# Optimization experiments

Hardware: AMD Instinct MI355X
Metric: run time of the kernel (lower is better)

## Reference

```python
import math
import jax, jax.numpy as jnp
import numpy as np

C = 32        # per-head dim
N_HEAD = 8
C_IN = 128

def setup_inputs() -> dict:
    key = jax.random.key(0)
    ks = jax.random.split(key, 10)
    B, S = 1, 256
    sc = 0.05  # keep logits in a sane range
    x    = jax.random.normal(ks[0], (B, S, S, C_IN), dtype=jnp.float32)
    bias = jax.random.normal(ks[1], (B, N_HEAD, S, S), dtype=jnp.float32)
    attention_mask = jax.random.randint(ks[2], (B, S, S), 0, 2).astype(bool)
    Wq = jax.random.normal(ks[3], (C_IN, C * N_HEAD), dtype=jnp.float32) * sc
    Wk = jax.random.normal(ks[4], (C_IN, C * N_HEAD), dtype=jnp.float32) * sc
    Wv = jax.random.normal(ks[5], (C_IN, C * N_HEAD), dtype=jnp.float32) * sc
    Wo = jax.random.normal(ks[6], (C * N_HEAD, C_IN), dtype=jnp.float32) * sc
    bo = jnp.zeros((C_IN,), dtype=jnp.float32)
    Wg = jax.random.normal(ks[7], (C_IN, C * N_HEAD), dtype=jnp.float32) * sc
    bg = jnp.zeros((C * N_HEAD,), dtype=jnp.float32)
    return {"x": x, "bias": bias, "attention_mask": attention_mask,
            "Wq": Wq, "Wk": Wk, "Wv": Wv, "Wo": Wo, "bo": bo, "Wg": Wg, "bg": bg}

def reference(x, bias, attention_mask, Wq, Wk, Wv, Wo, bo, Wg, bg):
    # x: [B, S, L, c_in]; attn_dim=2 is already the second-to-last dim,
    # so the torch movedim(attn_dim, -2) is the identity here.
    B, S, L, _ = x.shape
    q = x @ Wq  # [B, S, L, H*c]
    k = x @ Wk
    v = x @ Wv
    # split heads: [B, S, L, H, c] -> [B, S, H, L, c]
    def split_heads(t):
        return t.reshape(B, S, L, N_HEAD, C).transpose(0, 1, 3, 2, 4)
    q, k, v = split_heads(q), split_heads(k), split_heads(v)
    q = q / math.sqrt(C)
    # attention logits: [B, S, H, q, k]
    a = jnp.einsum('bshqc,bshkc->bshqk', q, k)
    # bias [B, H, q, k] -> broadcast over the axial batch dim S
    a = a + bias[:, None, :, :, :]
    # mask [B, S, k] -> [B, S, 1, 1, k]; masked positions get -inf
    m = attention_mask[:, :, None, None, :]
    a = jnp.where(m, a, -jnp.inf)
    a = jax.nn.softmax(a, axis=-1)
    o = jnp.einsum('bshqk,bshkc->bshqc', a, v)
    # merge heads: [B, S, H, L, c] -> [B, S, L, H*c]
    o = o.transpose(0, 1, 3, 2, 4).reshape(B, S, L, N_HEAD * C)
    # sigmoid gate
    g = jax.nn.sigmoid(x @ Wg + bg)
    o = g * o
    return o @ Wo + bo
```

## Files before the change

### kernel.cpp

```cpp
#include <hip/hip_runtime.h>
#include <hip/hip_bf16.h>
#include <cstdint>

#define CIN 128
#define NH 8
#define CH 32

typedef short bf16x8 __attribute__((ext_vector_type(8)));
typedef short bf16x4 __attribute__((ext_vector_type(4)));
typedef float f32x4 __attribute__((ext_vector_type(4)));

__device__ __forceinline__ short f2bf(float f) {
  union { float f; unsigned u; } v; v.f = f;
  unsigned r = (v.u + 0x7FFFu + ((v.u >> 16) & 1u)) >> 16;
  return (short)r;
}
__device__ __forceinline__ float bf2f(short s) {
  union { unsigned u; float f; } v; v.u = ((unsigned)(unsigned short)s) << 16;
  return v.f;
}
__device__ __forceinline__ unsigned pk2bf(float a, float b) {
  union { __hip_bfloat162 h; unsigned u; } cv;
  cv.h = __float22bfloat162_rn(make_float2(a, b));
  return cv.u;
}

__global__ __launch_bounds__(256) void prep(
    const float* __restrict__ Wq, const float* __restrict__ Wk,
    const float* __restrict__ Wv, const float* __restrict__ Wg,
    const float* __restrict__ Wo,
    const uint4* __restrict__ mask,
    short* __restrict__ WT, short* __restrict__ WoT,
    unsigned int* __restrict__ flag)
{
  __shared__ int viol;
  const int b = blockIdx.x;
  if (b < 64) {
    const float qscale = 0.17677669529663689f;
#pragma unroll
    for (int e = 0; e < 10; ++e) {
      int o = b * 2560 + e * 256 + threadIdx.x;
      if (o < 131072) {
        int n = o >> 7, k = o & 127;
        int seg = n >> 8, nn = n & 255;
        const float* W = (seg == 0) ? Wq : (seg == 1) ? Wk : (seg == 2) ? Wv : Wg;
        float v = W[k * 256 + nn];
        if (seg == 0) v *= qscale;
        WT[o] = f2bf(v);
      } else {
        int o2 = o - 131072;
        int n = o2 >> 8, k = o2 & 255;
        WoT[o2] = f2bf(Wo[k * 128 + n]);
      }
    }
  } else {
    if (threadIdx.x == 0) viol = 0;
    __syncthreads();
    int v = 0;
#pragma unroll
    for (int j = 0; j < 16; ++j) {
      uint4 w = mask[j * 256 + threadIdx.x];
      v |= (w.x > 1u) | (w.y > 1u) | (w.z > 1u) | (w.w > 1u);
    }
    if (v) atomicOr(&viol, 1);
    __syncthreads();
    if (threadIdx.x == 0) *flag = viol ? 0u : 1u;
  }
}

__global__ __launch_bounds__(512) void fused_attn(
    const float* __restrict__ x, const short* __restrict__ WT,
    const float* __restrict__ bias, const float* __restrict__ bg,
    const void* __restrict__ maskraw, const unsigned int* __restrict__ flagp,
    short* __restrict__ og)
{
  __shared__ __align__(16) short xl[256 * 136];
  __shared__ __align__(16) short kL[256 * 40];
  __shared__ __align__(16) short vL[32 * 264];
  __shared__ __align__(16) short qL[256 * 40];
  __shared__ __align__(16) short gL[256 * 40];
  __shared__ float lL[256];
  __shared__ unsigned int scratch[8];

  const int tid = threadIdx.x;
  const int srow = blockIdx.x;
  const int lane = tid & 63, w = tid >> 6;
  const int g = lane >> 4, c16 = lane & 15;
  const int myrow = w * 32;

  const unsigned int fl = *flagp;
  if (tid < 256) {
    int mv = fl ? ((const int*)maskraw)[srow * 256 + tid]
                : (int)((const unsigned char*)maskraw)[srow * 256 + tid];
    unsigned long long bb = __ballot(mv != 0);
    if (lane == 0) {
      scratch[w * 2 + 0] = (unsigned int)bb;
      scratch[w * 2 + 1] = (unsigned int)(bb >> 32);
    }
  }

  {
    const float* xs = x + (size_t)srow * 256 * 128;
#pragma unroll
    for (int it = 0; it < 16; ++it) {
      int idx = it * 512 + tid;
      int row = idx >> 5, c4 = idx & 31;
      float4 a = *(const float4*)(xs + (size_t)idx * 4);
      union { unsigned u[2]; bf16x4 v; } pu;
      pu.u[0] = pk2bf(a.x, a.y);
      pu.u[1] = pk2bf(a.z, a.w);
      *(bf16x4*)&xl[row * 136 + c4 * 4] = pu.v;
    }
  }
  __syncthreads();

  unsigned int mb[8];
#pragma unroll
  for (int j = 0; j < 8; ++j) mb[j] = scratch[j];

  const f32x4 zero4 = {0.f, 0.f, 0.f, 0.f};

#pragma unroll 1
  for (int h = 0; h < 8; ++h) {
    {
      f32x4 acc[2][2];
#pragma unroll
      for (int ct = 0; ct < 2; ++ct)
#pragma unroll
        for (int rt = 0; rt < 2; ++rt) acc[ct][rt] = zero4;
#pragma unroll
      for (int kk = 0; kk < 4; ++kk) {
        bf16x8 wf[2], xf[2];
#pragma unroll
        for (int ct = 0; ct < 2; ++ct)
          wf[ct] = *(const bf16x8*)(WT + (size_t)(256 + h * CH + ct * 16 + c16) * 128 + kk * 32 + g * 8);
#pragma unroll
        for (int rt = 0; rt < 2; ++rt)
          xf[rt] = *(const bf16x8*)&xl[(myrow + rt * 16 + c16) * 136 + kk * 32 + g * 8];
#pragma unroll
        for (int ct = 0; ct < 2; ++ct)
#pragma unroll
          for (int rt = 0; rt < 2; ++rt)
            acc[ct][rt] = __builtin_amdgcn_mfma_f32_16x16x32_bf16(wf[ct], xf[rt], acc[ct][rt], 0, 0, 0);
      }
#pragma unroll
      for (int ct = 0; ct < 2; ++ct)
#pragma unroll
        for (int rt = 0; rt < 2; ++rt) {
          union { unsigned u[2]; bf16x4 v; } pu;
          pu.u[0] = pk2bf(acc[ct][rt][0], acc[ct][rt][1]);
          pu.u[1] = pk2bf(acc[ct][rt][2], acc[ct][rt][3]);
          *(bf16x4*)&kL[(myrow + rt * 16 + c16) * 40 + ct * 16 + g * 4] = pu.v;
        }
    }
    {
      f32x4 acc[2][2];
#pragma unroll
      for (int rt = 0; rt < 2; ++rt)
#pragma unroll
        for (int ct = 0; ct < 2; ++ct) acc[rt][ct] = zero4;
#pragma unroll
      for (int kk = 0; kk < 4; ++kk) {
        bf16x8 wf[2], xf[2];
#pragma unroll
        for (int ct = 0; ct < 2; ++ct)
          wf[ct] = *(const bf16x8*)(WT + (size_t)(512 + h * CH + ct * 16 + c16) * 128 + kk * 32 + g * 8);
#pragma unroll
        for (int rt = 0; rt < 2; ++rt)
          xf[rt] = *(const bf16x8*)&xl[(myrow + rt * 16 + c16) * 136 + kk * 32 + g * 8];
#pragma unroll
        for (int rt = 0; rt < 2; ++rt)
#pragma unroll
          for (int ct = 0; ct < 2; ++ct)
            acc[rt][ct] = __builtin_amdgcn_mfma_f32_16x16x32_bf16(xf[rt], wf[ct], acc[rt][ct], 0, 0, 0);
      }
#pragma unroll
      for (int rt = 0; rt < 2; ++rt)
#pragma unroll
        for (int ct = 0; ct < 2; ++ct) {
          union { unsigned u[2]; bf16x4 v; } pu;
          pu.u[0] = pk2bf(acc[rt][ct][0], acc[rt][ct][1]);
          pu.u[1] = pk2bf(acc[rt][ct][2], acc[rt][ct][3]);
          *(bf16x4*)&vL[(ct * 16 + c16) * 264 + myrow + rt * 16 + g * 4] = pu.v;
        }
    }
    {
      f32x4 acc[2][2];
#pragma unroll
      for (int ct = 0; ct < 2; ++ct)
#pragma unroll
        for (int rt = 0; rt < 2; ++rt) acc[ct][rt] = zero4;
#pragma unroll
      for (int kk = 0; kk < 4; ++kk) {
        bf16x8 wf[2], xf[2];
#pragma unroll
        for (int ct = 0; ct < 2; ++ct)
          wf[ct] = *(const bf16x8*)(WT + (size_t)(0 + h * CH + ct * 16 + c16) * 128 + kk * 32 + g * 8);
#pragma unroll
        for (int rt = 0; rt < 2; ++rt)
          xf[rt] = *(const bf16x8*)&xl[(myrow + rt * 16 + c16) * 136 + kk * 32 + g * 8];
#pragma unroll
        for (int ct = 0; ct < 2; ++ct)
#pragma unroll
          for (int rt = 0; rt < 2; ++rt)
            acc[ct][rt] = __builtin_amdgcn_mfma_f32_16x16x32_bf16(wf[ct], xf[rt], acc[ct][rt], 0, 0, 0);
      }
#pragma unroll
      for (int ct = 0; ct < 2; ++ct)
#pragma unroll
        for (int rt = 0; rt < 2; ++rt) {
          union { unsigned u[2]; bf16x4 v; } pu;
          pu.u[0] = pk2bf(acc[ct][rt][0], acc[ct][rt][1]);
          pu.u[1] = pk2bf(acc[ct][rt][2], acc[ct][rt][3]);
          *(bf16x4*)&qL[(myrow + rt * 16 + c16) * 40 + ct * 16 + g * 4] = pu.v;
        }
    }
    {
      f32x4 acc[2][2];
#pragma unroll
      for (int ct = 0; ct < 2; ++ct)
#pragma unroll
        for (int rt = 0; rt < 2; ++rt) acc[ct][rt] = zero4;
#pragma unroll
      for (int kk = 0; kk < 4; ++kk) {
        bf16x8 wf[2], xf[2];
#pragma unroll
        for (int ct = 0; ct < 2; ++ct)
          wf[ct] = *(const bf16x8*)(WT + (size_t)(768 + h * CH + ct * 16 + c16) * 128 + kk * 32 + g * 8);
#pragma unroll
        for (int rt = 0; rt < 2; ++rt)
          xf[rt] = *(const bf16x8*)&xl[(myrow + rt * 16 + c16) * 136 + kk * 32 + g * 8];
#pragma unroll
        for (int ct = 0; ct < 2; ++ct)
#pragma unroll
          for (int rt = 0; rt < 2; ++rt)
            acc[ct][rt] = __builtin_amdgcn_mfma_f32_16x16x32_bf16(wf[ct], xf[rt], acc[ct][rt], 0, 0, 0);
      }
#pragma unroll
      for (int ct = 0; ct < 2; ++ct) {
        float4 bgv = *(const float4*)(bg + h * CH + ct * 16 + g * 4);
#pragma unroll
        for (int rt = 0; rt < 2; ++rt) {
          float v0 = 1.f / (1.f + __expf(-(acc[ct][rt][0] + bgv.x)));
          float v1 = 1.f / (1.f + __expf(-(acc[ct][rt][1] + bgv.y)));
          float v2 = 1.f / (1.f + __expf(-(acc[ct][rt][2] + bgv.z)));
          float v3 = 1.f / (1.f + __expf(-(acc[ct][rt][3] + bgv.w)));
          union { unsigned u[2]; bf16x4 v; } pu;
          pu.u[0] = pk2bf(v0, v1);
          pu.u[1] = pk2bf(v2, v3);
          *(bf16x4*)&gL[(myrow + rt * 16 + c16) * 40 + ct * 16 + g * 4] = pu.v;
        }
      }
    }
    __syncthreads();

    const int qb = myrow;
    bf16x8 qf[2];
#pragma unroll
    for (int qt = 0; qt < 2; ++qt)
      qf[qt] = *(const bf16x8*)&qL[(qb + qt * 16 + c16) * 40 + g * 8];

    float l_[2] = {0.f, 0.f};
    f32x4 O[2][2];
#pragma unroll
    for (int qt = 0; qt < 2; ++qt) { O[qt][0] = zero4; O[qt][1] = zero4; }

    const float* bh = bias + (size_t)h * 65536;

#pragma unroll 1
    for (int ch = 0; ch < 8; ++ch) {
      float4 bb4[2][2];
#pragma unroll
      for (int kt = 0; kt < 2; ++kt)
#pragma unroll
        for (int qt = 0; qt < 2; ++qt)
          bb4[kt][qt] = *(const float4*)(bh + (size_t)(qb + qt * 16 + c16) * 256 +
                                         ch * 32 + kt * 16 + g * 4);

#pragma unroll
      for (int kt = 0; kt < 2; ++kt) {
        bf16x8 kf = *(const bf16x8*)&kL[(ch * 32 + kt * 16 + c16) * 40 + g * 8];
        bf16x4 vlo = *(const bf16x4*)&vL[(size_t)c16 * 264 + ch * 32 + kt * 16 + g * 4];
        bf16x4 vhi = *(const bf16x4*)&vL[(size_t)(16 + c16) * 264 + ch * 32 + kt * 16 + g * 4];
        const unsigned nib = (mb[ch] >> (kt * 16 + g * 4)) & 0xFu;
        float em[4];
#pragma unroll
        for (int i = 0; i < 4; ++i) em[i] = ((nib >> i) & 1u) ? 1.f : 0.f;
#pragma unroll
        for (int qt = 0; qt < 2; ++qt) {
          f32x4 S = __builtin_amdgcn_mfma_f32_16x16x32_bf16(kf, qf[qt], zero4, 0, 0, 0);
          float p0 = em[0] * __expf(fminf(S[0] + bb4[kt][qt].x, 85.f));
          float p1 = em[1] * __expf(fminf(S[1] + bb4[kt][qt].y, 85.f));
          float p2 = em[2] * __expf(fminf(S[2] + bb4[kt][qt].z, 85.f));
          float p3 = em[3] * __expf(fminf(S[3] + bb4[kt][qt].w, 85.f));
          l_[qt] += (p0 + p1) + (p2 + p3);
          union { unsigned u[2]; bf16x4 v; } pu;
          pu.u[0] = pk2bf(p0, p1);
          pu.u[1] = pk2bf(p2, p3);
          O[qt][0] = __builtin_amdgcn_mfma_f32_16x16x16bf16_1k(pu.v, vlo, O[qt][0], 0, 0, 0);
          O[qt][1] = __builtin_amdgcn_mfma_f32_16x16x16bf16_1k(pu.v, vhi, O[qt][1], 0, 0, 0);
        }
      }
    }

#pragma unroll
    for (int qt = 0; qt < 2; ++qt) {
      float v = l_[qt];
      v += __shfl_xor(v, 16);
      v += __shfl_xor(v, 32);
      if (lane < 16) lL[myrow + qt * 16 + c16] = v;
    }

#pragma unroll
    for (int qt = 0; qt < 2; ++qt)
#pragma unroll
      for (int i = 0; i < 4; ++i) {
        float l = lL[myrow + qt * 16 + g * 4 + i];
        float inv = 1.f / l;
        int row = qb + qt * 16 + g * 4 + i;
        short* orow = og + ((size_t)srow * 256 + row) * 256 + h * CH;
#pragma unroll
        for (int half = 0; half < 2; ++half) {
          int c = half * 16 + c16;
          float gv = bf2f(gL[row * 40 + c]);
          orow[c] = f2bf(O[qt][half][i] * inv * gv);
        }
      }
    __syncthreads();
  }
}

__global__ __launch_bounds__(256) void out_proj(
    const short* __restrict__ og, const short* __restrict__ WoT,
    const float* __restrict__ bo, float* __restrict__ out)
{
  __shared__ short Al[64 * 136];
  __shared__ short Bl[128 * 136];
  const int tid = threadIdx.x;
  const int lane = tid & 63, w = tid >> 6;
  const int g = lane >> 4, c16 = lane & 15;
  const int wr = w & 1, wc = w >> 1;
  const int row0 = blockIdx.x * 64;

  f32x4 acc[2][4];
#pragma unroll
  for (int rt = 0; rt < 2; ++rt)
#pragma unroll
    for (int ct = 0; ct < 4; ++ct) acc[rt][ct] = (f32x4){0.f, 0.f, 0.f, 0.f};

  for (int kk0 = 0; kk0 < 256; kk0 += 128) {
#pragma unroll
    for (int ch = 0; ch < 4; ++ch) {
      int c = ch * 256 + tid;
      int r = c >> 4, kc = c & 15;
      *(bf16x8*)&Al[r * 136 + kc * 8] =
          *(const bf16x8*)(og + (size_t)(row0 + r) * 256 + kk0 + kc * 8);
    }
#pragma unroll
    for (int ch = 0; ch < 8; ++ch) {
      int c = ch * 256 + tid;
      int r = c >> 4, kc = c & 15;
      *(bf16x8*)&Bl[r * 136 + kc * 8] =
          *(const bf16x8*)(WoT + (size_t)r * 256 + kk0 + kc * 8);
    }
    __syncthreads();
#pragma unroll
    for (int kk = 0; kk < 4; ++kk) {
      bf16x8 af[2], bfr[4];
#pragma unroll
      for (int rt = 0; rt < 2; ++rt)
        af[rt] = *(const bf16x8*)&Al[(wr * 32 + rt * 16 + c16) * 136 + kk * 32 + g * 8];
#pragma unroll
      for (int ct = 0; ct < 4; ++ct)
        bfr[ct] = *(const bf16x8*)&Bl[(wc * 64 + ct * 16 + c16) * 136 + kk * 32 + g * 8];
#pragma unroll
      for (int rt = 0; rt < 2; ++rt)
#pragma unroll
        for (int ct = 0; ct < 4; ++ct)
          acc[rt][ct] = __builtin_amdgcn_mfma_f32_16x16x32_bf16(af[rt], bfr[ct], acc[rt][ct], 0, 0, 0);
    }
    __syncthreads();
  }

#pragma unroll
  for (int rt = 0; rt < 2; ++rt)
#pragma unroll
    for (int ct = 0; ct < 4; ++ct) {
      int col = wc * 64 + ct * 16 + c16;
      float bv = bo[col];
#pragma unroll
      for (int i = 0; i < 4; ++i) {
        int row = row0 + wr * 32 + rt * 16 + g * 4 + i;
        out[(size_t)row * CIN + col] = acc[rt][ct][i] + bv;
      }
    }
}

extern "C" void kernel_launch(void* const* d_in, const int* in_sizes, int n_in,
                              void* d_out, int out_size, void* d_ws, size_t ws_size,
                              hipStream_t stream) {
  const float* x    = (const float*)d_in[0];
  const float* bias = (const float*)d_in[1];
  const void*  mask = d_in[2];
  const float* Wq   = (const float*)d_in[3];
  const float* Wk   = (const float*)d_in[4];
  const float* Wv   = (const float*)d_in[5];
  const float* Wo   = (const float*)d_in[6];
  const float* bo   = (const float*)d_in[7];
  const float* Wg   = (const float*)d_in[8];
  const float* bg   = (const float*)d_in[9];
  float* out = (float*)d_out;

  unsigned int* flag = (unsigned int*)d_ws;
  short* WT  = (short*)((char*)d_ws + 256);
  short* WoT = WT + 131072;
  short* og  = WoT + 32768;

  prep<<<65, 256, 0, stream>>>(Wq, Wk, Wv, Wg, Wo, (const uint4*)mask,
                               WT, WoT, flag);
  fused_attn<<<256, 512, 0, stream>>>(x, WT, bias, bg, mask, flag, og);
  out_proj<<<1024, 256, 0, stream>>>(og, WoT, bo, out);
}
```

Measured before the change: 245.7 us.

## Fuse output projection into attention kernel, accumulating per-head Wo contributions

```diff
diff --git a/kernel.cpp b/kernel.cpp
--- a/kernel.cpp
+++ b/kernel.cpp
@@ -70,15 +70,16 @@
 
 __global__ __launch_bounds__(512) void fused_attn(
     const float* __restrict__ x, const short* __restrict__ WT,
+    const short* __restrict__ WoT,
     const float* __restrict__ bias, const float* __restrict__ bg,
+    const float* __restrict__ bo,
     const void* __restrict__ maskraw, const unsigned int* __restrict__ flagp,
-    short* __restrict__ og)
+    float* __restrict__ out)
 {
   __shared__ __align__(16) short xl[256 * 136];
   __shared__ __align__(16) short kL[256 * 40];
   __shared__ __align__(16) short vL[32 * 264];
   __shared__ __align__(16) short qL[256 * 40];
-  __shared__ __align__(16) short gL[256 * 40];
   __shared__ float lL[256];
   __shared__ unsigned int scratch[8];
 
@@ -119,9 +120,15 @@
   for (int j = 0; j < 8; ++j) mb[j] = scratch[j];
 
   const f32x4 zero4 = {0.f, 0.f, 0.f, 0.f};
+  f32x4 acc_out[2][8];
+#pragma unroll
+  for (int qt = 0; qt < 2; ++qt)
+#pragma unroll
+    for (int ct = 0; ct < 8; ++ct) acc_out[qt][ct] = zero4;
 
 #pragma unroll 1
   for (int h = 0; h < 8; ++h) {
+    f32x4 ga[2][2];
     {
       f32x4 acc[2][2];
 #pragma unroll
@@ -181,7 +188,7 @@
           union { unsigned u[2]; bf16x4 v; } pu;
           pu.u[0] = pk2bf(acc[rt][ct][0], acc[rt][ct][1]);
           pu.u[1] = pk2bf(acc[rt][ct][2], acc[rt][ct][3]);
-          *(bf16x4*)&vL[(ct * 16 + c16) * 264 + myrow + rt * 16 + g * 4] = pu.v;
+          *(bf16x4*)&vL[(size_t)(ct * 16 + c16) * 264 + myrow + rt * 16 + g * 4] = pu.v;
         }
     }
     {
@@ -216,11 +223,10 @@
         }
     }
     {
-      f32x4 acc[2][2];
-#pragma unroll
-      for (int ct = 0; ct < 2; ++ct)
-#pragma unroll
-        for (int rt = 0; rt < 2; ++rt) acc[ct][rt] = zero4;
+#pragma unroll
+      for (int rt = 0; rt < 2; ++rt)
+#pragma unroll
+        for (int ct = 0; ct < 2; ++ct) ga[rt][ct] = zero4;
 #pragma unroll
       for (int kk = 0; kk < 4; ++kk) {
         bf16x8 wf[2], xf[2];
@@ -231,25 +237,10 @@
         for (int rt = 0; rt < 2; ++rt)
           xf[rt] = *(const bf16x8*)&xl[(myrow + rt * 16 + c16) * 136 + kk * 32 + g * 8];
 #pragma unroll
-        for (int ct = 0; ct < 2; ++ct)
-#pragma unroll
-          for (int rt = 0; rt < 2; ++rt)
-            acc[ct][rt] = __builtin_amdgcn_mfma_f32_16x16x32_bf16(wf[ct], xf[rt], acc[ct][rt], 0, 0, 0);
-      }
-#pragma unroll
-      for (int ct = 0; ct < 2; ++ct) {
-        float4 bgv = *(const float4*)(bg + h * CH + ct * 16 + g * 4);
-#pragma unroll
-        for (int rt = 0; rt < 2; ++rt) {
-          float v0 = 1.f / (1.f + __expf(-(acc[ct][rt][0] + bgv.x)));
-          float v1 = 1.f / (1.f + __expf(-(acc[ct][rt][1] + bgv.y)));
-          float v2 = 1.f / (1.f + __expf(-(acc[ct][rt][2] + bgv.z)));
-          float v3 = 1.f / (1.f + __expf(-(acc[ct][rt][3] + bgv.w)));
-          union { unsigned u[2]; bf16x4 v; } pu;
-          pu.u[0] = pk2bf(v0, v1);
-          pu.u[1] = pk2bf(v2, v3);
-          *(bf16x4*)&gL[(myrow + rt * 16 + c16) * 40 + ct * 16 + g * 4] = pu.v;
-        }
+        for (int rt = 0; rt < 2; ++rt)
+#pragma unroll
+          for (int ct = 0; ct < 2; ++ct)
+            ga[rt][ct] = __builtin_amdgcn_mfma_f32_16x16x32_bf16(xf[rt], wf[ct], ga[rt][ct], 0, 0, 0);
       }
     }
     __syncthreads();
@@ -311,89 +302,48 @@
       if (lane < 16) lL[myrow + qt * 16 + c16] = v;
     }
 
+    {
+      float bgl0 = bg[h * CH + c16];
+      float bgl1 = bg[h * CH + 16 + c16];
+#pragma unroll
+      for (int qt = 0; qt < 2; ++qt)
+#pragma unroll
+        for (int i = 0; i < 4; ++i) {
+          int row = qb + qt * 16 + g * 4 + i;
+          float inv = 1.f / lL[myrow + qt * 16 + g * 4 + i];
+          float g0 = 1.f / (1.f + __expf(-(ga[qt][0][i] + bgl0)));
+          float g1 = 1.f / (1.f + __expf(-(ga[qt][1][i] + bgl1)));
+          qL[row * 40 + c16]      = f2bf(O[qt][0][i] * inv * g0);
+          qL[row * 40 + 16 + c16] = f2bf(O[qt][1][i] * inv * g1);
+        }
+    }
+
+    {
+      bf16x8 wo[8];
+#pragma unroll
+      for (int ct = 0; ct < 8; ++ct)
+        wo[ct] = *(const bf16x8*)(WoT + (size_t)(ct * 16 + c16) * 256 + h * 32 + g * 8);
+#pragma unroll
+      for (int qt = 0; qt < 2; ++qt) {
+        bf16x8 of = *(const bf16x8*)&qL[(qb + qt * 16 + c16) * 40 + g * 8];
+#pragma unroll
+        for (int ct = 0; ct < 8; ++ct)
+          acc_out[qt][ct] = __builtin_amdgcn_mfma_f32_16x16x32_bf16(of, wo[ct], acc_out[qt][ct], 0, 0, 0);
+      }
+    }
+    __syncthreads();
+  }
+
+#pragma unroll
+  for (int ct = 0; ct < 8; ++ct) {
+    float bv = bo[ct * 16 + c16];
 #pragma unroll
     for (int qt = 0; qt < 2; ++qt)
 #pragma unroll
-      for (int i = 0; i < 4; ++i) {
-        float l = lL[myrow + qt * 16 + g * 4 + i];
-        float inv = 1.f / l;
-        int row = qb + qt * 16 + g * 4 + i;
-        short* orow = og + ((size_t)srow * 256 + row) * 256 + h * CH;
-#pragma unroll
-        for (int half = 0; half < 2; ++half) {
-          int c = half * 16 + c16;
-          float gv = bf2f(gL[row * 40 + c]);
-          orow[c] = f2bf(O[qt][half][i] * inv * gv);
-        }
-      }
-    __syncthreads();
-  }
-}
-
-__global__ __launch_bounds__(256) void out_proj(
-    const short* __restrict__ og, const short* __restrict__ WoT,
-    const float* __restrict__ bo, float* __restrict__ out)
-{
-  __shared__ short Al[64 * 136];
-  __shared__ short Bl[128 * 136];
-  const int tid = threadIdx.x;
-  const int lane = tid & 63, w = tid >> 6;
-  const int g = lane >> 4, c16 = lane & 15;
-  const int wr = w & 1, wc = w >> 1;
-  const int row0 = blockIdx.x * 64;
-
-  f32x4 acc[2][4];
-#pragma unroll
-  for (int rt = 0; rt < 2; ++rt)
-#pragma unroll
-    for (int ct = 0; ct < 4; ++ct) acc[rt][ct] = (f32x4){0.f, 0.f, 0.f, 0.f};
-
-  for (int kk0 = 0; kk0 < 256; kk0 += 128) {
-#pragma unroll
-    for (int ch = 0; ch < 4; ++ch) {
-      int c = ch * 256 + tid;
-      int r = c >> 4, kc = c & 15;
-      *(bf16x8*)&Al[r * 136 + kc * 8] =
-          *(const bf16x8*)(og + (size_t)(row0 + r) * 256 + kk0 + kc * 8);
-    }
-#pragma unroll
-    for (int ch = 0; ch < 8; ++ch) {
-      int c = ch * 256 + tid;
-      int r = c >> 4, kc = c & 15;
-      *(bf16x8*)&Bl[r * 136 + kc * 8] =
-          *(const bf16x8*)(WoT + (size_t)r * 256 + kk0 + kc * 8);
-    }
-    __syncthreads();
-#pragma unroll
-    for (int kk = 0; kk < 4; ++kk) {
-      bf16x8 af[2], bfr[4];
-#pragma unroll
-      for (int rt = 0; rt < 2; ++rt)
-        af[rt] = *(const bf16x8*)&Al[(wr * 32 + rt * 16 + c16) * 136 + kk * 32 + g * 8];
-#pragma unroll
-      for (int ct = 0; ct < 4; ++ct)
-        bfr[ct] = *(const bf16x8*)&Bl[(wc * 64 + ct * 16 + c16) * 136 + kk * 32 + g * 8];
-#pragma unroll
-      for (int rt = 0; rt < 2; ++rt)
-#pragma unroll
-        for (int ct = 0; ct < 4; ++ct)
-          acc[rt][ct] = __builtin_amdgcn_mfma_f32_16x16x32_bf16(af[rt], bfr[ct], acc[rt][ct], 0, 0, 0);
-    }
-    __syncthreads();
-  }
-
-#pragma unroll
-  for (int rt = 0; rt < 2; ++rt)
-#pragma unroll
-    for (int ct = 0; ct < 4; ++ct) {
-      int col = wc * 64 + ct * 16 + c16;
-      float bv = bo[col];
-#pragma unroll
-      for (int i = 0; i < 4; ++i) {
-        int row = row0 + wr * 32 + rt * 16 + g * 4 + i;
-        out[(size_t)row * CIN + col] = acc[rt][ct][i] + bv;
-      }
-    }
+      for (int i = 0; i < 4; ++i)
+        out[((size_t)srow * 256 + myrow + qt * 16 + g * 4 + i) * 128 + ct * 16 + c16] =
+            acc_out[qt][ct][i] + bv;
+  }
 }
 
 extern "C" void kernel_launch(void* const* d_in, const int* in_sizes, int n_in,
@@ -414,10 +364,9 @@
   unsigned int* flag = (unsigned int*)d_ws;
   short* WT  = (short*)((char*)d_ws + 256);
   short* WoT = WT + 131072;
-  short* og  = WoT + 32768;
 
   prep<<<65, 256, 0, stream>>>(Wq, Wk, Wv, Wg, Wo, (const uint4*)mask,
                                WT, WoT, flag);
-  fused_attn<<<256, 512, 0, stream>>>(x, WT, bias, bg, mask, flag, og);
-  out_proj<<<1024, 256, 0, stream>>>(og, WoT, bo, out);
-}
+  fused_attn<<<256, 512, 0, stream>>>(x, WT, WoT, bias, bg, bo,
+                                      mask, flag, out);
+}
```

After: 242.5 us. About the same (-1.3%).
